# Performance work log

Measured on AMD Instinct MI355X. Metric: run time of the kernel, lower is better.

The kernel has to match this reference:

```python
import jax, jax.numpy as jnp
import numpy as np

N = 50000   # num nodes
D = 2       # sheaf stalk dim (final_d == d, no hp/lp)
HC = 128    # hidden channels
E0 = 200000 # undirected edges (stored in both directions -> 2*E0 directed)


def setup_inputs() -> dict:
    key = jax.random.key(0)
    k = jax.random.split(key, 6)
    x = jax.random.normal(k[0], (N * D, HC), dtype=jnp.float32)
    src = jax.random.randint(k[1], (E0,), 0, N, dtype=jnp.int32)
    dst = jax.random.randint(k[2], (E0,), 0, N, dtype=jnp.int32)
    W_sheaf = jax.random.normal(k[3], (D, 2 * D * HC), dtype=jnp.float32) * 0.05
    W_left = jax.random.normal(k[4], (D, D), dtype=jnp.float32) * 0.3
    W_right = jax.random.normal(k[5], (HC, HC), dtype=jnp.float32) * (1.0 / np.sqrt(HC))
    t = jnp.zeros((1,), dtype=jnp.float32)
    return {"t": t, "x": x, "src": src, "dst": dst,
            "W_sheaf": W_sheaf, "W_left": W_left, "W_right": W_right}


def reference(t, x, src, dst, W_sheaf, W_left, W_right):
    # Directed edge list: each undirected edge appears in both directions;
    # edge i and edge i+E0 are reverses of each other.
    row = jnp.concatenate([src, dst])  # [E]
    col = jnp.concatenate([dst, src])  # [E]
    e0 = src.shape[0]
    rev = jnp.concatenate([jnp.arange(e0) + e0, jnp.arange(e0)])

    # --- Sheaf learner (LocalConcatSheafLearner, diag maps) ---
    x_maps = x.reshape(N, D * HC)                      # node features for learner
    Wa, Wb = W_sheaf[:, : D * HC], W_sheaf[:, D * HC:]
    # tanh(Linear(cat(x_row, x_col))) without materializing the concat
    maps = jnp.tanh(x_maps[row] @ Wa.T + x_maps[col] @ Wb.T)  # [E, D]

    # --- DiagLaplacianBuilder (normalised, augmented) ---
    off = -maps * maps[rev]                                   # off-diag block (row,col): -F_e_row * F_e_col
    diag = jax.ops.segment_sum(maps ** 2, row, num_segments=N)  # [N, D]
    dis = 1.0 / jnp.sqrt(diag + 1.0)                          # augmented degree^-1/2
    off = dis[row] * off * dis[col]
    diag = dis * diag * dis

    # --- left weights: act on the d-block axis ---
    xl = (x.T.reshape(-1, D)) @ W_left.T                      # [HC*N, D]
    x = xl.reshape(HC, N * D).T                               # [N*D, HC]

    # --- right weights: act on channels ---
    x = x @ W_right.T

    # --- spmm(L, -x): block-diagonal-per-d sheaf Laplacian ---
    xb = (-x).reshape(N, D, HC)
    y = diag[..., None] * xb + jax.ops.segment_sum(off[..., None] * xb[col], row, num_segments=N)
    return y.reshape(N * D, HC)
```

## Files before the change

### kernel.cpp

```cpp
#include <hip/hip_runtime.h>

static constexpr int kN   = 50000;
static constexpr int kNR  = 100000;
static constexpr int kE0  = 200000;
static constexpr int kE2  = 400000;
static constexpr int kCAP = 32;

typedef _Float16 f16;
typedef f16   f16x8 __attribute__((ext_vector_type(8)));
typedef f16   f16x4 __attribute__((ext_vector_type(4)));
typedef float f32x4 __attribute__((ext_vector_type(4)));

__global__ __launch_bounds__(256) void k_node(
    const float* __restrict__ x, const float* __restrict__ Wsh,
    const float* __restrict__ Wl, const float* __restrict__ Wr,
    f16* __restrict__ xb, float4* __restrict__ ab)
{
    __shared__ f16 Bl[128][136];
    __shared__ f16 Al[64][136];

    const int t   = threadIdx.x;
    const int blk = blockIdx.x;

    const float wl00 = Wl[0], wl01 = Wl[1], wl10 = Wl[2], wl11 = Wl[3];

    #pragma unroll
    for (int i = 0; i < 64; ++i) {
        int idx = i * 256 + t;
        Bl[idx >> 7][idx & 127] = (f16)Wr[idx];
    }

    const int w = t >> 6, lane = t & 63;

    #pragma unroll
    for (int i = 0; i < 8; ++i) {
        const int f4   = i * 256 + t;
        const int row  = f4 >> 5;
        const int h4   = (f4 & 31) << 2;
        const int grow = blk * 64 + row;
        float4 xo = make_float4(0.f, 0.f, 0.f, 0.f);
        float4 xp = xo;
        if (grow < kNR) {
            xo = *(const float4*)(x + (size_t)grow * 128 + h4);
            xp = *(const float4*)(x + (size_t)(grow ^ 1) * 128 + h4);
        }
        const int dp = row & 1;
        const float  c0 = dp ? wl10 : wl00;
        const float  c1 = dp ? wl11 : wl01;
        const float4 x0 = dp ? xp : xo;
        const float4 x1 = dp ? xo : xp;
        Al[row][h4 + 0] = (f16)(c0 * x0.x + c1 * x1.x);
        Al[row][h4 + 1] = (f16)(c0 * x0.y + c1 * x1.y);
        Al[row][h4 + 2] = (f16)(c0 * x0.z + c1 * x1.z);
        Al[row][h4 + 3] = (f16)(c0 * x0.w + c1 * x1.w);

        const int kb = dp * 128 + h4;
        const float4 wa0 = *(const float4*)(Wsh + kb);
        const float4 wb0 = *(const float4*)(Wsh + 256 + kb);
        const float4 wa1 = *(const float4*)(Wsh + 512 + kb);
        const float4 wb1 = *(const float4*)(Wsh + 768 + kb);
        float pa0 = xo.x*wa0.x + xo.y*wa0.y + xo.z*wa0.z + xo.w*wa0.w;
        float pa1 = xo.x*wa1.x + xo.y*wa1.y + xo.z*wa1.z + xo.w*wa1.w;
        float pb0 = xo.x*wb0.x + xo.y*wb0.y + xo.z*wb0.z + xo.w*wb0.w;
        float pb1 = xo.x*wb1.x + xo.y*wb1.y + xo.z*wb1.z + xo.w*wb1.w;
        #pragma unroll
        for (int o = 32; o > 0; o >>= 1) {
            pa0 += __shfl_xor(pa0, o);
            pa1 += __shfl_xor(pa1, o);
            pb0 += __shfl_xor(pb0, o);
            pb1 += __shfl_xor(pb1, o);
        }
        if (lane == 0) {
            const int node = blk * 32 + i * 4 + w;
            if (node < kN) ab[node] = make_float4(pa0, pa1, pb0, pb1);
        }
    }
    __syncthreads();

    const int lr = lane & 15, lk = lane >> 4;
    f16x8 afr[4];
    #pragma unroll
    for (int kk = 0; kk < 4; ++kk)
        afr[kk] = *(const f16x8*)&Al[16 * w + lr][kk * 32 + lk * 8];

    f32x4 accs[8];
    #pragma unroll
    for (int j = 0; j < 8; ++j) {
        f32x4 acc = {0.f, 0.f, 0.f, 0.f};
        #pragma unroll
        for (int kk = 0; kk < 4; ++kk) {
            f16x8 bfr = *(const f16x8*)&Bl[j * 16 + lr][kk * 32 + lk * 8];
            acc = __builtin_amdgcn_mfma_f32_16x16x32_f16(afr[kk], bfr, acc, 0, 0, 0);
        }
        accs[j] = acc;
    }

    __syncthreads();
    #pragma unroll
    for (int j = 0; j < 8; ++j) {
        #pragma unroll
        for (int r = 0; r < 4; ++r)
            Al[16 * w + lk * 4 + r][j * 16 + lr] = (f16)(-accs[j][r]);
    }
    __syncthreads();

    const int orow  = 16 * w + (lane >> 2);
    const int grow0 = blk * 64 + orow;
    if (grow0 < kNR) {
        const int q = lane & 3;
        f16* dst = xb + (size_t)grow0 * 128 + q * 32;
        #pragma unroll
        for (int cch = 0; cch < 4; ++cch)
            *(f16x8*)(dst + cch * 8) = *(const f16x8*)&Al[orow][q * 32 + cch * 8];
    }
}

__global__ __launch_bounds__(256) void k_edge1(
    const int* __restrict__ src, const int* __restrict__ dst,
    const float4* __restrict__ ab, float2* __restrict__ maps2,
    int* __restrict__ cnt, int2* __restrict__ adj)
{
    const int j = blockIdx.x * 256 + threadIdx.x;
    if (j >= kE2) return;
    const bool fwd = j < kE0;
    const int o = fwd ? j : j - kE0;
    const int s = src[o], d = dst[o];
    const int row = fwd ? s : d;
    const int col = fwd ? d : s;
    const float4 ar = ab[row], ac = ab[col];
    const float m0 = tanhf(ar.x + ac.z);
    const float m1 = tanhf(ar.y + ac.w);
    maps2[j] = make_float2(m0, m1);
    const int p = atomicAdd(&cnt[row], 1);
    if (p < kCAP) adj[(size_t)row * kCAP + p] = make_int2(j, col);
}

__global__ __launch_bounds__(256) void k_diag(
    const int* __restrict__ cnt, const int2* __restrict__ adj,
    const float2* __restrict__ maps2, float2* __restrict__ diag)
{
    const int n = blockIdx.x * 256 + threadIdx.x;
    if (n >= kN) return;
    int c = cnt[n];
    if (c > kCAP) c = kCAP;
    const int2* al = adj + (size_t)n * kCAP;
    float s0 = 0.f, s1 = 0.f;
    for (int k = 0; k < c; k += 4) {
        const int4 ea = *(const int4*)(al + k);
        const int4 eb = *(const int4*)(al + k + 2);
        const bool v1 = (k + 1 < c), v2 = (k + 2 < c), v3 = (k + 3 < c);
        const int j0 = ea.x;
        const int j1 = v1 ? ea.z : ea.x;
        const int j2 = v2 ? eb.x : ea.x;
        const int j3 = v3 ? eb.z : ea.x;
        const float2 m0 = maps2[j0], m1 = maps2[j1];
        const float2 m2 = maps2[j2], m3 = maps2[j3];
        const float w1 = v1 ? 1.f : 0.f, w2 = v2 ? 1.f : 0.f, w3 = v3 ? 1.f : 0.f;
        s0 += m0.x*m0.x + w1*m1.x*m1.x + w2*m2.x*m2.x + w3*m3.x*m3.x;
        s1 += m0.y*m0.y + w1*m1.y*m1.y + w2*m2.y*m2.y + w3*m3.y*m3.y;
    }
    diag[n] = make_float2(s0, s1);
}

__global__ __launch_bounds__(256) void k_off(
    const int* __restrict__ src, const int* __restrict__ dst,
    const float2* __restrict__ maps2, const float2* __restrict__ diag,
    float2* __restrict__ off)
{
    const int j = blockIdx.x * 256 + threadIdx.x;
    if (j >= kE0) return;
    const float2 ma = maps2[j];
    const float2 mb = maps2[j + kE0];
    const int s = src[j], d = dst[j];
    const float2 ds = diag[s], dt = diag[d];
    off[j] = make_float2(-ma.x * mb.x * rsqrtf((ds.x + 1.0f) * (dt.x + 1.0f)),
                         -ma.y * mb.y * rsqrtf((ds.y + 1.0f) * (dt.y + 1.0f)));
}

__global__ __launch_bounds__(256) void k_gather(
    const f16* __restrict__ xb, const float* __restrict__ diag,
    const float2* __restrict__ off, const int* __restrict__ cnt,
    const int2* __restrict__ adj, float* __restrict__ y)
{
    const int node = blockIdx.x * 4 + (threadIdx.x >> 6);
    const int lane = threadIdx.x & 63;
    const int d    = lane >> 5;
    const int h4   = (lane & 31) << 2;
    const size_t rowoff = ((size_t)node * 2 + d) * 128 + h4;
    const f16x4 own = *(const f16x4*)(xb + rowoff);
    const float dv  = diag[node * 2 + d];
    const float dg  = dv / (dv + 1.0f);
    f32x4 acc = {dg * (float)own[0], dg * (float)own[1],
                 dg * (float)own[2], dg * (float)own[3]};
    int c = cnt[node];
    if (c > kCAP) c = kCAP;
    const int2* al = adj + (size_t)node * kCAP;

    for (int k = 0; k < c; k += 8) {
        const int4 ea = *(const int4*)(al + k);
        const int4 eb = *(const int4*)(al + k + 2);
        const int4 ec = *(const int4*)(al + k + 4);
        const int4 ed = *(const int4*)(al + k + 6);
        int  jj[8] = {ea.x, ea.z, eb.x, eb.z, ec.x, ec.z, ed.x, ed.z};
        int  nn[8] = {ea.y, ea.w, eb.y, eb.w, ec.y, ec.w, ed.y, ed.w};
        bool vv[8];
        #pragma unroll
        for (int i = 0; i < 8; ++i) {
            vv[i] = (k + i < c);
            jj[i] = vv[i] ? jj[i] : ea.x;
            nn[i] = vv[i] ? nn[i] : ea.y;
        }
        float2 qq[8];
        f16x4  ww[8];
        #pragma unroll
        for (int i = 0; i < 8; ++i) {
            const int oe = jj[i] - (jj[i] >= kE0 ? kE0 : 0);
            qq[i] = off[oe];
            ww[i] = *(const f16x4*)(xb + ((size_t)nn[i] * 2 + d) * 128 + h4);
        }
        #pragma unroll
        for (int i = 0; i < 8; ++i) {
            const float o = vv[i] ? (d ? qq[i].y : qq[i].x) : 0.0f;
            acc[0] += o * (float)ww[i][0];
            acc[1] += o * (float)ww[i][1];
            acc[2] += o * (float)ww[i][2];
            acc[3] += o * (float)ww[i][3];
        }
    }
    __builtin_nontemporal_store(acc, (f32x4*)(y + rowoff));
}

extern "C" void kernel_launch(void* const* d_in, const int* in_sizes, int n_in,
                              void* d_out, int out_size, void* d_ws, size_t ws_size,
                              hipStream_t stream)
{
    const float* x   = (const float*)d_in[1];
    const int*   src = (const int*)d_in[2];
    const int*   dst = (const int*)d_in[3];
    const float* Wsh = (const float*)d_in[4];
    const float* Wl  = (const float*)d_in[5];
    const float* Wr  = (const float*)d_in[6];

    char* ws = (char*)d_ws;
    f16*    xb    = (f16*)   (ws + 0);
    float4* ab    = (float4*)(ws + 25600000);
    float2* maps2 = (float2*)(ws + 26400000);
    float2* off   = (float2*)(ws + 29600000);
    float2* diag  = (float2*)(ws + 31200000);
    int*    cnt   = (int*)   (ws + 31600000);
    int2*   adj   = (int2*)  (ws + 31800000);

    (void)hipMemsetAsync(cnt, 0, 200000, stream);

    k_node  <<<1563, 256, 0, stream>>>(x, Wsh, Wl, Wr, xb, ab);
    k_edge1 <<<1563, 256, 0, stream>>>(src, dst, ab, maps2, cnt, adj);
    k_diag  <<<196,  256, 0, stream>>>(cnt, adj, maps2, diag);
    k_off   <<<782,  256, 0, stream>>>(src, dst, maps2, diag, off);
    k_gather<<<12500, 256, 0, stream>>>(xb, (const float*)diag, off, cnt, adj, (float*)d_out);
}
```

Baseline: 133.4 us.

## Pre-convert W_right to fp16 and pad adjacency lists with sentinel zero edges

```diff
diff --git a/kernel.cpp b/kernel.cpp
--- a/kernel.cpp
+++ b/kernel.cpp
@@ -11,24 +11,24 @@
 typedef f16   f16x4 __attribute__((ext_vector_type(4)));
 typedef float f32x4 __attribute__((ext_vector_type(4)));
 
+__global__ __launch_bounds__(256) void k_wrh(
+    const float* __restrict__ Wr, f16* __restrict__ Wrh)
+{
+    const int i = blockIdx.x * 256 + threadIdx.x;
+    Wrh[i] = (f16)Wr[i];
+}
+
 __global__ __launch_bounds__(256) void k_node(
     const float* __restrict__ x, const float* __restrict__ Wsh,
-    const float* __restrict__ Wl, const float* __restrict__ Wr,
+    const float* __restrict__ Wl, const f16* __restrict__ Wrh,
     f16* __restrict__ xb, float4* __restrict__ ab)
 {
-    __shared__ f16 Bl[128][136];
     __shared__ f16 Al[64][136];
 
     const int t   = threadIdx.x;
     const int blk = blockIdx.x;
 
     const float wl00 = Wl[0], wl01 = Wl[1], wl10 = Wl[2], wl11 = Wl[3];
-
-    #pragma unroll
-    for (int i = 0; i < 64; ++i) {
-        int idx = i * 256 + t;
-        Bl[idx >> 7][idx & 127] = (f16)Wr[idx];
-    }
 
     const int w = t >> 6, lane = t & 63;
 
@@ -89,7 +89,7 @@
         f32x4 acc = {0.f, 0.f, 0.f, 0.f};
         #pragma unroll
         for (int kk = 0; kk < 4; ++kk) {
-            f16x8 bfr = *(const f16x8*)&Bl[j * 16 + lr][kk * 32 + lk * 8];
+            const f16x8 bfr = *(const f16x8*)(Wrh + (size_t)(j * 16 + lr) * 128 + kk * 32 + lk * 8);
             acc = __builtin_amdgcn_mfma_f32_16x16x32_f16(afr[kk], bfr, acc, 0, 0, 0);
         }
         accs[j] = acc;
@@ -136,14 +136,14 @@
 }
 
 __global__ __launch_bounds__(256) void k_diag(
-    const int* __restrict__ cnt, const int2* __restrict__ adj,
+    const int* __restrict__ cnt, int2* __restrict__ adj,
     const float2* __restrict__ maps2, float2* __restrict__ diag)
 {
     const int n = blockIdx.x * 256 + threadIdx.x;
     if (n >= kN) return;
     int c = cnt[n];
     if (c > kCAP) c = kCAP;
-    const int2* al = adj + (size_t)n * kCAP;
+    int2* al = adj + (size_t)n * kCAP;
     float s0 = 0.f, s1 = 0.f;
     for (int k = 0; k < c; k += 4) {
         const int4 ea = *(const int4*)(al + k);
@@ -159,6 +159,8 @@
         s0 += m0.x*m0.x + w1*m1.x*m1.x + w2*m2.x*m2.x + w3*m3.x*m3.x;
         s1 += m0.y*m0.y + w1*m1.y*m1.y + w2*m2.y*m2.y + w3*m3.y*m3.y;
     }
+    const int cpad = (c + 7) & ~7;
+    for (int k = c; k < cpad; ++k) al[k] = make_int2(kE2, n);
     diag[n] = make_float2(s0, s1);
 }
 
@@ -168,7 +170,11 @@
     float2* __restrict__ off)
 {
     const int j = blockIdx.x * 256 + threadIdx.x;
-    if (j >= kE0) return;
+    if (j >= kE0) {
+        if (j == kE0) off[kE0] = make_float2(0.f, 0.f);
+        return;
+    }
+    if (j == 0) off[kE0] = make_float2(0.f, 0.f);
     const float2 ma = maps2[j];
     const float2 mb = maps2[j + kE0];
     const int s = src[j], d = dst[j];
@@ -201,15 +207,8 @@
         const int4 eb = *(const int4*)(al + k + 2);
         const int4 ec = *(const int4*)(al + k + 4);
         const int4 ed = *(const int4*)(al + k + 6);
-        int  jj[8] = {ea.x, ea.z, eb.x, eb.z, ec.x, ec.z, ed.x, ed.z};
-        int  nn[8] = {ea.y, ea.w, eb.y, eb.w, ec.y, ec.w, ed.y, ed.w};
-        bool vv[8];
-        #pragma unroll
-        for (int i = 0; i < 8; ++i) {
-            vv[i] = (k + i < c);
-            jj[i] = vv[i] ? jj[i] : ea.x;
-            nn[i] = vv[i] ? nn[i] : ea.y;
-        }
+        const int jj[8] = {ea.x, ea.z, eb.x, eb.z, ec.x, ec.z, ed.x, ed.z};
+        const int nn[8] = {ea.y, ea.w, eb.y, eb.w, ec.y, ec.w, ed.y, ed.w};
         float2 qq[8];
         f16x4  ww[8];
         #pragma unroll
@@ -220,7 +219,7 @@
         }
         #pragma unroll
         for (int i = 0; i < 8; ++i) {
-            const float o = vv[i] ? (d ? qq[i].y : qq[i].x) : 0.0f;
+            const float o = d ? qq[i].y : qq[i].x;
             acc[0] += o * (float)ww[i][0];
             acc[1] += o * (float)ww[i][1];
             acc[2] += o * (float)ww[i][2];
@@ -246,15 +245,17 @@
     float4* ab    = (float4*)(ws + 25600000);
     float2* maps2 = (float2*)(ws + 26400000);
     float2* off   = (float2*)(ws + 29600000);
-    float2* diag  = (float2*)(ws + 31200000);
-    int*    cnt   = (int*)   (ws + 31600000);
-    int2*   adj   = (int2*)  (ws + 31800000);
+    float2* diag  = (float2*)(ws + 31200016);
+    int*    cnt   = (int*)   (ws + 31600016);
+    int2*   adj   = (int2*)  (ws + 31800016);
+    f16*    Wrh   = (f16*)   (ws + 44600016);
 
     (void)hipMemsetAsync(cnt, 0, 200000, stream);
 
-    k_node  <<<1563, 256, 0, stream>>>(x, Wsh, Wl, Wr, xb, ab);
+    k_wrh   <<<64,   256, 0, stream>>>(Wr, Wrh);
+    k_node  <<<1563, 256, 0, stream>>>(x, Wsh, Wl, Wrh, xb, ab);
     k_edge1 <<<1563, 256, 0, stream>>>(src, dst, ab, maps2, cnt, adj);
     k_diag  <<<196,  256, 0, stream>>>(cnt, adj, maps2, diag);
-    k_off   <<<782,  256, 0, stream>>>(src, dst, maps2, diag, off);
+    k_off   <<<783,  256, 0, stream>>>(src, dst, maps2, diag, off);
     k_gather<<<12500, 256, 0, stream>>>(xb, (const float*)diag, off, cnt, adj, (float*)d_out);
 }
```

Result: slower. 174.9 us (+31.1%).
